# Kernel optimization log

Measured on AMD Instinct MI355X. Metric: run time of the kernel, lower is better.

The kernel has to match this reference:

```python
import jax, jax.numpy as jnp
from jax import lax
import numpy as np

WINDOW_SIZE = 11
SIGMA = 1.5
C1 = 0.01 ** 2
C2 = 0.03 ** 2


def _gauss_1d(n=WINDOW_SIZE, sigma=SIGMA):
    # replicates cv2.getGaussianKernel(n, sigma)
    x = np.arange(n, dtype=np.float64) - (n - 1) / 2.0
    g = np.exp(-(x ** 2) / (2.0 * sigma ** 2))
    return (g / g.sum()).astype(np.float32)


def _blur(x, g):
    """Separable 2D Gaussian blur of x [N,1,H,W]; math equals conv with g g^T."""
    p = g.shape[0] // 2
    kh = g.reshape(1, 1, -1, 1).astype(x.dtype)  # [O,I,KH,1]
    kw = g.reshape(1, 1, 1, -1).astype(x.dtype)  # [O,I,1,KW]
    dn = ('NCHW', 'OIHW', 'NCHW')
    x = lax.conv_general_dilated(x, kh, (1, 1), [(p, p), (0, 0)], dimension_numbers=dn)
    x = lax.conv_general_dilated(x, kw, (1, 1), [(0, 0), (p, p)], dimension_numbers=dn)
    return x


def _ssim_loss_2d(a, b):
    """a, b: [N,1,H,W]. Returns 1 - mean(SSIM map) with the module's exact formula."""
    g = jnp.asarray(_gauss_1d())
    mu1 = _blur(a, g)
    mu2 = _blur(b, g)
    mu1_sq = mu1 * mu1
    mu2_sq = mu2 * mu2
    mu1_mu2 = mu1 * mu2
    sigma1_sq = _blur(a * a, g) - mu1_sq
    sigma2_sq = _blur(b * b, g) - mu2_sq
    sigma12 = _blur(a * b, g) - mu1_mu2
    luminance = (2 * mu1_mu2 + C1) / (mu1_sq + mu2_sq + C1)
    contrast = (2 * sigma12 + C2) / (sigma1_sq + sigma2_sq + C2)
    structure = (sigma12 + C2) / (jnp.sqrt(sigma1_sq) * jnp.sqrt(sigma2_sq) + C2)
    ssim = luminance * contrast * structure
    return 1.0 - ssim.mean()


def setup_inputs() -> dict:
    key = jax.random.key(0)
    k1, k2, k3 = jax.random.split(key, 3)
    img1_3d = jax.random.uniform(k1, (4, 1, 16, 512, 512), dtype=jnp.float32)
    img1_2d = jax.random.uniform(k2, (4, 1, 512, 512), dtype=jnp.float32)
    img2 = jax.random.uniform(k3, (4, 1, 16, 512, 512), dtype=jnp.float32)
    return {"img1_3d": img1_3d, "img1_2d": img1_2d, "img2": img2}


def reference(img1_3d, img1_2d, img2):
    B, C, D, H, W = img1_3d.shape  # C == 1 (forced by groups=C with single-out-channel weight)
    # 3D SSIM: kernel depth 1, depth padding 0 -> per-slice 2D blur; fold D into batch.
    a3 = img1_3d.reshape(B * D, 1, H, W)
    b3 = img2.reshape(B * D, 1, H, W)
    loss3d = _ssim_loss_2d(a3, b3)
    # 2D SSIM against depth-averaged img2.
    b2 = jnp.mean(img2, axis=2)  # [B,1,H,W]
    loss2d = _ssim_loss_2d(img1_2d, b2)
    return loss3d + loss2d
```

## Files before the change

### kernel.cpp

```cpp
#include <hip/hip_runtime.h>
#include <cmath>


#define WSZ 11
#define IMG 512
#define SLICE (IMG * IMG)

typedef float f32x2 __attribute__((ext_vector_type(2)));
typedef float f32x4 __attribute__((ext_vector_type(4)));

struct G11 { float w[WSZ]; };

__global__ __launch_bounds__(256, 5)
void ssim_pk_kernel(const float* __restrict__ A3, const float* __restrict__ B3,
                    const float* __restrict__ A2, const float* __restrict__ B2,
                    double* __restrict__ acc, G11 gw)
{
    __shared__ f32x4 A4[2][262];
    __shared__ f32x4 B4[2][262];
    __shared__ f32x2 Z2[2][262];
    __shared__ float bsum[4];

    const int tx = threadIdx.x;
    const int x0 = tx * 2;

    const int unit = blockIdx.x;
    const float* Ap;
    const float* Bp;
    double* accp;
    int y0, TST;
    if (unit < 1536) {
        int slice = unit / 24;
        int band  = unit - slice * 24;
        Ap = A3 + (long)slice * SLICE;
        Bp = B3 + (long)slice * SLICE;
        accp = acc + 0;
        if (band < 16) { y0 = band * 22;              TST = 22 + 10; }
        else           { y0 = 352 + (band - 16) * 20; TST = 20 + 10; }
    } else {
        int uu = unit - 1536;
        int img  = uu >> 6;
        int band = uu & 63;
        Ap = A2 + (long)img * SLICE;
        Bp = B2 + (long)img * SLICE;
        accp = acc + 1;
        y0 = band * 8;
        TST = 8 + 10;
    }

    if (tx < 3) {
        f32x4 z4 = {0.f, 0.f, 0.f, 0.f};
        f32x2 z2 = {0.f, 0.f};
        A4[0][tx] = z4; A4[1][tx] = z4; A4[0][259 + tx] = z4; A4[1][259 + tx] = z4;
        B4[0][tx] = z4; B4[1][tx] = z4; B4[0][259 + tx] = z4; B4[1][259 + tx] = z4;
        Z2[0][tx] = z2; Z2[1][tx] = z2; Z2[0][259 + tx] = z2; Z2[1][259 + tx] = z2;
    }

    f32x2 ra[11], rb[11];
    #pragma unroll
    for (int i = 0; i < 11; i++) { ra[i] = (f32x2){0.f, 0.f}; rb[i] = (f32x2){0.f, 0.f}; }

    float sum = 0.f;

    f32x2 aN = {0.f, 0.f}, bN = {0.f, 0.f};
    {
        int r = y0 - 5;
        if (r >= 0 && r < IMG) {
            aN = *(const f32x2*)&Ap[(long)r * IMG + x0];
            bN = *(const f32x2*)&Bp[(long)r * IMG + x0];
        }
    }

    const f32x2 C1v = {1e-4f, 1e-4f};
    const f32x2 C2v = {9e-4f, 9e-4f};

    for (int t0 = 0; t0 < TST; t0 += 11) {
        #pragma unroll
        for (int u = 0; u < 11; u++) {
            const int t = t0 + u;
            if (t < TST) {
                ra[u] = aN;
                rb[u] = bN;

                {
                    int rn = y0 - 4 + t;
                    aN = (f32x2){0.f, 0.f}; bN = (f32x2){0.f, 0.f};
                    if ((t + 1 < TST) && rn >= 0 && rn < IMG) {
                        aN = *(const f32x2*)&Ap[(long)rn * IMG + x0];
                        bN = *(const f32x2*)&Bp[(long)rn * IMG + x0];
                    }
                }

                if (t >= 10) {
                    f32x2 m1 = {0.f, 0.f}, m2 = m1, xx = m1, yy = m1, zz = m1;
                    #pragma unroll
                    for (int j = 0; j < 11; j++) {
                        const int s = (u + 1 + j) % 11;
                        const f32x2 g2 = {gw.w[j], gw.w[j]};
                        f32x2 a = ra[s], b = rb[s];
                        f32x2 ga = g2 * a, gb = g2 * b;
                        m1 += ga; m2 += gb;
                        xx += ga * a; yy += gb * b; zz += ga * b;
                    }
                    const int buf = t & 1;
                    A4[buf][3 + tx] = __builtin_shufflevector(m1, m2, 0, 1, 2, 3);
                    B4[buf][3 + tx] = __builtin_shufflevector(xx, yy, 0, 1, 2, 3);
                    Z2[buf][3 + tx] = zz;
                    __syncthreads();

                    f32x2 OM1 = {0.f, 0.f}, OM2 = OM1, OXX = OM1, OYY = OM1, OZZ = OM1;
                    {
                        f32x4 pa = A4[buf][tx], pb = B4[buf][tx];
                        f32x2 pz = Z2[buf][tx];
                        const f32x2 c = {gw.w[0], 0.f};
                        OM1 += c * __builtin_shufflevector(pa, pa, 1, 1);
                        OM2 += c * __builtin_shufflevector(pa, pa, 3, 3);
                        OXX += c * __builtin_shufflevector(pb, pb, 1, 1);
                        OYY += c * __builtin_shufflevector(pb, pb, 3, 3);
                        OZZ += c * __builtin_shufflevector(pz, pz, 1, 1);
                    }
                    #pragma unroll
                    for (int jj = 1; jj <= 5; jj++) {
                        f32x4 pa = A4[buf][tx + jj], pb = B4[buf][tx + jj];
                        f32x2 pz = Z2[buf][tx + jj];
                        const f32x2 cA = {gw.w[2 * jj - 1], gw.w[2 * jj - 2]};
                        const f32x2 cB = {gw.w[2 * jj],     gw.w[2 * jj - 1]};
                        OM1 += cA * __builtin_shufflevector(pa, pa, 0, 0)
                             + cB * __builtin_shufflevector(pa, pa, 1, 1);
                        OM2 += cA * __builtin_shufflevector(pa, pa, 2, 2)
                             + cB * __builtin_shufflevector(pa, pa, 3, 3);
                        OXX += cA * __builtin_shufflevector(pb, pb, 0, 0)
                             + cB * __builtin_shufflevector(pb, pb, 1, 1);
                        OYY += cA * __builtin_shufflevector(pb, pb, 2, 2)
                             + cB * __builtin_shufflevector(pb, pb, 3, 3);
                        OZZ += cA * __builtin_shufflevector(pz, pz, 0, 0)
                             + cB * __builtin_shufflevector(pz, pz, 1, 1);
                    }
                    {
                        f32x4 pa = A4[buf][tx + 6], pb = B4[buf][tx + 6];
                        f32x2 pz = Z2[buf][tx + 6];
                        const f32x2 c = {0.f, gw.w[10]};
                        OM1 += c * __builtin_shufflevector(pa, pa, 0, 0);
                        OM2 += c * __builtin_shufflevector(pa, pa, 2, 2);
                        OXX += c * __builtin_shufflevector(pb, pb, 0, 0);
                        OYY += c * __builtin_shufflevector(pb, pb, 2, 2);
                        OZZ += c * __builtin_shufflevector(pz, pz, 0, 0);
                    }

                    f32x2 m1s = OM1 * OM1, m2s = OM2 * OM2, m12 = OM1 * OM2;
                    f32x2 s1 = OXX - m1s, s2 = OYY - m2s, s12 = OZZ - m12;
                    f32x2 d1 = m1s + m2s + C1v;
                    f32x2 d2 = s1 + s2 + C2v;
                    f32x2 num = (2.f * m12 + C1v) * (2.f * s12 + C2v) * (s12 + C2v);
                    float d3x = __builtin_amdgcn_sqrtf(s1.x) * __builtin_amdgcn_sqrtf(s2.x) + 9e-4f;
                    float d3y = __builtin_amdgcn_sqrtf(s1.y) * __builtin_amdgcn_sqrtf(s2.y) + 9e-4f;
                    sum += num.x * __builtin_amdgcn_rcpf(d1.x * d2.x * d3x);
                    sum += num.y * __builtin_amdgcn_rcpf(d1.y * d2.y * d3y);
                }
            }
        }
    }

    for (int off = 32; off > 0; off >>= 1)
        sum += __shfl_down(sum, off, 64);
    if ((tx & 63) == 0) bsum[tx >> 6] = sum;
    __syncthreads();
    if (tx == 0) {
        float tot = bsum[0] + bsum[1] + bsum[2] + bsum[3];
        atomicAdd(accp, (double)tot);
    }
}

__global__ __launch_bounds__(256) void depth_mean4_kernel(
    const float4* __restrict__ img2, float4* __restrict__ b2)
{
    const int per = SLICE / 4;
    int idx = blockIdx.x * 256 + threadIdx.x;
    int b = idx >> 16;
    int p = idx & (per - 1);
    const float4* src = img2 + (long)b * 16 * per + p;
    float sx = 0.f, sy = 0.f, sz = 0.f, sw = 0.f;
    #pragma unroll
    for (int d = 0; d < 16; d++) {
        float4 v = src[(long)d * per];
        sx += v.x; sy += v.y; sz += v.z; sw += v.w;
    }
    float4 o; o.x = sx * 0.0625f; o.y = sy * 0.0625f; o.z = sz * 0.0625f; o.w = sw * 0.0625f;
    b2[idx] = o;
}

__global__ void finalize_kernel(const double* __restrict__ acc, float* __restrict__ out)
{
    double loss3 = 1.0 - acc[0] / (64.0 * (double)SLICE);
    double loss2 = 1.0 - acc[1] / (4.0 * (double)SLICE);
    out[0] = (float)(loss3 + loss2);
}

extern "C" void kernel_launch(void* const* d_in, const int* in_sizes, int n_in,
                              void* d_out, int out_size, void* d_ws, size_t ws_size,
                              hipStream_t stream)
{
    const float* img1_3d = (const float*)d_in[0];
    const float* img1_2d = (const float*)d_in[1];
    const float* img2    = (const float*)d_in[2];
    float* out = (float*)d_out;

    double* acc = (double*)d_ws;
    float*  b2  = (float*)((char*)d_ws + 256);

    G11 gw;
    {
        double g[WSZ], s = 0.0;
        for (int i = 0; i < WSZ; i++) {
            double xx = (double)i - (WSZ - 1) / 2.0;
            g[i] = std::exp(-(xx * xx) / (2.0 * 1.5 * 1.5));
            s += g[i];
        }
        for (int i = 0; i < WSZ; i++) gw.w[i] = (float)(g[i] / s);
    }

    hipMemsetAsync(acc, 0, 2 * sizeof(double), stream);

    depth_mean4_kernel<<<(4 * SLICE / 4) / 256, 256, 0, stream>>>(
        (const float4*)img2, (float4*)b2);

    ssim_pk_kernel<<<1792, 256, 0, stream>>>(img1_3d, img2, img1_2d, b2, acc, gw);

    finalize_kernel<<<1, 1, 0, stream>>>(acc, out);
}
```

Measured before the change: 106.0 us.

## Make each wavefront own an independent column strip to drop block barriers

Restructures the SSIM kernel so each 64-lane wavefront processes its own 58-column output strip with 3-column halos, using per-wave shared buffers instead of a block-wide row. This removes the per-row __syncthreads and the double-buffered LDS, relying on intra-wavefront ordering of LDS accesses. The cost is redundant halo loads and compute (6 of 64 lanes produce no output) and more atomics, one per wave. Band partitioning for the 3D and 2D parts is also rebalanced.

```diff
diff --git a/kernel.cpp b/kernel.cpp
--- a/kernel.cpp
+++ b/kernel.cpp
@@ -12,48 +12,55 @@
 struct G11 { float w[WSZ]; };
 
 __global__ __launch_bounds__(256, 5)
-void ssim_pk_kernel(const float* __restrict__ A3, const float* __restrict__ B3,
+void ssim_ws_kernel(const float* __restrict__ A3, const float* __restrict__ B3,
                     const float* __restrict__ A2, const float* __restrict__ B2,
                     double* __restrict__ acc, G11 gw)
 {
-    __shared__ f32x4 A4[2][262];
-    __shared__ f32x4 B4[2][262];
-    __shared__ f32x2 Z2[2][262];
-    __shared__ float bsum[4];
-
-    const int tx = threadIdx.x;
-    const int x0 = tx * 2;
-
-    const int unit = blockIdx.x;
-    const float* Ap;
-    const float* Bp;
-    double* accp;
-    int y0, TST;
-    if (unit < 1536) {
-        int slice = unit / 24;
-        int band  = unit - slice * 24;
+    __shared__ f32x4 A4[4][70];
+    __shared__ f32x4 B4[4][70];
+    __shared__ f32x2 Z2[4][70];
+
+    const int tx   = threadIdx.x;
+    const int wid  = tx >> 6;
+    const int lane = tx & 63;
+
+    const int u = blockIdx.x * 4 + wid;
+    const float* Ap; const float* Bp; double* accp;
+    int y0, BND, strip;
+    if (u < 7680) {
+        int slice = u / 120;
+        int r = u - slice * 120;
+        int band = r / 5; strip = r - band * 5;
         Ap = A3 + (long)slice * SLICE;
         Bp = B3 + (long)slice * SLICE;
         accp = acc + 0;
-        if (band < 16) { y0 = band * 22;              TST = 22 + 10; }
-        else           { y0 = 352 + (band - 16) * 20; TST = 20 + 10; }
+        if (band < 8) { y0 = band * 22;              BND = 22; }
+        else          { y0 = 176 + (band - 8) * 21;  BND = 21; }
     } else {
-        int uu = unit - 1536;
-        int img  = uu >> 6;
-        int band = uu & 63;
+        int u2 = u - 7680;
+        int img = u2 / 130;
+        int r2 = u2 - img * 130;
+        int band = r2 / 5; strip = r2 - band * 5;
         Ap = A2 + (long)img * SLICE;
         Bp = B2 + (long)img * SLICE;
         accp = acc + 1;
-        y0 = band * 8;
-        TST = 8 + 10;
-    }
-
-    if (tx < 3) {
-        f32x4 z4 = {0.f, 0.f, 0.f, 0.f};
-        f32x2 z2 = {0.f, 0.f};
-        A4[0][tx] = z4; A4[1][tx] = z4; A4[0][259 + tx] = z4; A4[1][259 + tx] = z4;
-        B4[0][tx] = z4; B4[1][tx] = z4; B4[0][259 + tx] = z4; B4[1][259 + tx] = z4;
-        Z2[0][tx] = z2; Z2[1][tx] = z2; Z2[0][259 + tx] = z2; Z2[1][259 + tx] = z2;
+        if (band < 18) { y0 = band * 20;              BND = 20; }
+        else           { y0 = 360 + (band - 18) * 19; BND = 19; }
+    }
+    const int TST = BND + 10;
+    const int ip  = strip * 58 - 3 + lane;
+    const bool vin  = (ip >= 0) && (ip < 256);
+    const bool vout = (lane >= 3) && (lane <= 60) && (ip < 256);
+    const int x0 = 2 * ip;
+
+    if (lane < 3) {
+        A4[wid][lane] = (f32x4){0.f, 0.f, 0.f, 0.f};
+        B4[wid][lane] = (f32x4){0.f, 0.f, 0.f, 0.f};
+        Z2[wid][lane] = (f32x2){0.f, 0.f};
+    } else if (lane >= 61) {
+        A4[wid][lane + 6] = (f32x4){0.f, 0.f, 0.f, 0.f};
+        B4[wid][lane + 6] = (f32x4){0.f, 0.f, 0.f, 0.f};
+        Z2[wid][lane + 6] = (f32x2){0.f, 0.f};
     }
 
     f32x2 ra[11], rb[11];
@@ -65,7 +72,7 @@
     f32x2 aN = {0.f, 0.f}, bN = {0.f, 0.f};
     {
         int r = y0 - 5;
-        if (r >= 0 && r < IMG) {
+        if (r >= 0 && r < IMG && vin) {
             aN = *(const f32x2*)&Ap[(long)r * IMG + x0];
             bN = *(const f32x2*)&Bp[(long)r * IMG + x0];
         }
@@ -76,16 +83,16 @@
 
     for (int t0 = 0; t0 < TST; t0 += 11) {
         #pragma unroll
-        for (int u = 0; u < 11; u++) {
-            const int t = t0 + u;
+        for (int uu = 0; uu < 11; uu++) {
+            const int t = t0 + uu;
             if (t < TST) {
-                ra[u] = aN;
-                rb[u] = bN;
+                ra[uu] = aN;
+                rb[uu] = bN;
 
                 {
                     int rn = y0 - 4 + t;
                     aN = (f32x2){0.f, 0.f}; bN = (f32x2){0.f, 0.f};
-                    if ((t + 1 < TST) && rn >= 0 && rn < IMG) {
+                    if ((t + 1 < TST) && rn >= 0 && rn < IMG && vin) {
                         aN = *(const f32x2*)&Ap[(long)rn * IMG + x0];
                         bN = *(const f32x2*)&Bp[(long)rn * IMG + x0];
                     }
@@ -95,23 +102,21 @@
                     f32x2 m1 = {0.f, 0.f}, m2 = m1, xx = m1, yy = m1, zz = m1;
                     #pragma unroll
                     for (int j = 0; j < 11; j++) {
-                        const int s = (u + 1 + j) % 11;
+                        const int s = (uu + 1 + j) % 11;
                         const f32x2 g2 = {gw.w[j], gw.w[j]};
                         f32x2 a = ra[s], b = rb[s];
                         f32x2 ga = g2 * a, gb = g2 * b;
                         m1 += ga; m2 += gb;
                         xx += ga * a; yy += gb * b; zz += ga * b;
                     }
-                    const int buf = t & 1;
-                    A4[buf][3 + tx] = __builtin_shufflevector(m1, m2, 0, 1, 2, 3);
-                    B4[buf][3 + tx] = __builtin_shufflevector(xx, yy, 0, 1, 2, 3);
-                    Z2[buf][3 + tx] = zz;
-                    __syncthreads();
+                    A4[wid][lane + 3] = __builtin_shufflevector(m1, m2, 0, 1, 2, 3);
+                    B4[wid][lane + 3] = __builtin_shufflevector(xx, yy, 0, 1, 2, 3);
+                    Z2[wid][lane + 3] = zz;
 
                     f32x2 OM1 = {0.f, 0.f}, OM2 = OM1, OXX = OM1, OYY = OM1, OZZ = OM1;
                     {
-                        f32x4 pa = A4[buf][tx], pb = B4[buf][tx];
-                        f32x2 pz = Z2[buf][tx];
+                        f32x4 pa = A4[wid][lane], pb = B4[wid][lane];
+                        f32x2 pz = Z2[wid][lane];
                         const f32x2 c = {gw.w[0], 0.f};
                         OM1 += c * __builtin_shufflevector(pa, pa, 1, 1);
                         OM2 += c * __builtin_shufflevector(pa, pa, 3, 3);
@@ -121,8 +126,8 @@
                     }
                     #pragma unroll
                     for (int jj = 1; jj <= 5; jj++) {
-                        f32x4 pa = A4[buf][tx + jj], pb = B4[buf][tx + jj];
-                        f32x2 pz = Z2[buf][tx + jj];
+                        f32x4 pa = A4[wid][lane + jj], pb = B4[wid][lane + jj];
+                        f32x2 pz = Z2[wid][lane + jj];
                         const f32x2 cA = {gw.w[2 * jj - 1], gw.w[2 * jj - 2]};
                         const f32x2 cB = {gw.w[2 * jj],     gw.w[2 * jj - 1]};
                         OM1 += cA * __builtin_shufflevector(pa, pa, 0, 0)
@@ -137,8 +142,8 @@
                              + cB * __builtin_shufflevector(pz, pz, 1, 1);
                     }
                     {
-                        f32x4 pa = A4[buf][tx + 6], pb = B4[buf][tx + 6];
-                        f32x2 pz = Z2[buf][tx + 6];
+                        f32x4 pa = A4[wid][lane + 6], pb = B4[wid][lane + 6];
+                        f32x2 pz = Z2[wid][lane + 6];
                         const f32x2 c = {0.f, gw.w[10]};
                         OM1 += c * __builtin_shufflevector(pa, pa, 0, 0);
                         OM2 += c * __builtin_shufflevector(pa, pa, 2, 2);
@@ -154,8 +159,9 @@
                     f32x2 num = (2.f * m12 + C1v) * (2.f * s12 + C2v) * (s12 + C2v);
                     float d3x = __builtin_amdgcn_sqrtf(s1.x) * __builtin_amdgcn_sqrtf(s2.x) + 9e-4f;
                     float d3y = __builtin_amdgcn_sqrtf(s1.y) * __builtin_amdgcn_sqrtf(s2.y) + 9e-4f;
-                    sum += num.x * __builtin_amdgcn_rcpf(d1.x * d2.x * d3x);
-                    sum += num.y * __builtin_amdgcn_rcpf(d1.y * d2.y * d3y);
+                    float contrib = num.x * __builtin_amdgcn_rcpf(d1.x * d2.x * d3x)
+                                  + num.y * __builtin_amdgcn_rcpf(d1.y * d2.y * d3y);
+                    sum += vout ? contrib : 0.f;
                 }
             }
         }
@@ -163,12 +169,8 @@
 
     for (int off = 32; off > 0; off >>= 1)
         sum += __shfl_down(sum, off, 64);
-    if ((tx & 63) == 0) bsum[tx >> 6] = sum;
-    __syncthreads();
-    if (tx == 0) {
-        float tot = bsum[0] + bsum[1] + bsum[2] + bsum[3];
-        atomicAdd(accp, (double)tot);
-    }
+    if (lane == 0)
+        atomicAdd(accp, (double)sum);
 }
 
 __global__ __launch_bounds__(256) void depth_mean4_kernel(
@@ -224,7 +226,7 @@
     depth_mean4_kernel<<<(4 * SLICE / 4) / 256, 256, 0, stream>>>(
         (const float4*)img2, (float4*)b2);
 
-    ssim_pk_kernel<<<1792, 256, 0, stream>>>(img1_3d, img2, img1_2d, b2, acc, gw);
+    ssim_ws_kernel<<<2050, 256, 0, stream>>>(img1_3d, img2, img1_2d, b2, acc, gw);
 
     finalize_kernel<<<1, 1, 0, stream>>>(acc, out);
 }
```

Result: slower. 166.7 us (+57.3%).

## Fuse depth-mean into SSIM kernel and schedule 2D blocks first

Applied to the files above, without the earlier changes.

Removes the separate depth_mean kernel and its intermediate buffer. The 2D SSIM blocks now average the 16 depth slices of img2 on the fly for each row they load. Those blocks are moved to the front of the grid so their heavier loads start early and overlap with the 3D blocks. This saves a kernel launch and a write-then-read of the averaged image. In exchange, each 2D block issues 16x the B loads, and halo rows are re-averaged across overlapping bands.

```diff
diff --git a/kernel.cpp b/kernel.cpp
--- a/kernel.cpp
+++ b/kernel.cpp
@@ -13,7 +13,7 @@
 
 __global__ __launch_bounds__(256, 5)
 void ssim_pk_kernel(const float* __restrict__ A3, const float* __restrict__ B3,
-                    const float* __restrict__ A2, const float* __restrict__ B2,
+                    const float* __restrict__ A2,
                     double* __restrict__ acc, G11 gw)
 {
     __shared__ f32x4 A4[2][262];
@@ -25,28 +25,38 @@
     const int x0 = tx * 2;
 
     const int unit = blockIdx.x;
+    const bool m16 = (unit < 256);
     const float* Ap;
     const float* Bp;
     double* accp;
     int y0, TST;
-    if (unit < 1536) {
-        int slice = unit / 24;
-        int band  = unit - slice * 24;
+    if (m16) {
+        int img  = unit >> 6;
+        int band = unit & 63;
+        Ap = A2 + (long)img * SLICE;
+        Bp = B3 + (long)img * 16 * SLICE;
+        accp = acc + 1;
+        y0 = band * 8;
+        TST = 8 + 10;
+    } else {
+        int uu = unit - 256;
+        int slice = uu / 24;
+        int band  = uu - slice * 24;
         Ap = A3 + (long)slice * SLICE;
         Bp = B3 + (long)slice * SLICE;
         accp = acc + 0;
         if (band < 16) { y0 = band * 22;              TST = 22 + 10; }
         else           { y0 = 352 + (band - 16) * 20; TST = 20 + 10; }
-    } else {
-        int uu = unit - 1536;
-        int img  = uu >> 6;
-        int band = uu & 63;
-        Ap = A2 + (long)img * SLICE;
-        Bp = B2 + (long)img * SLICE;
-        accp = acc + 1;
-        y0 = band * 8;
-        TST = 8 + 10;
-    }
+    }
+
+    auto loadB = [&](int r) -> f32x2 {
+        if (!m16) return *(const f32x2*)&Bp[(long)r * IMG + x0];
+        f32x2 s = {0.f, 0.f};
+        #pragma unroll
+        for (int d = 0; d < 16; d++)
+            s += *(const f32x2*)&Bp[(long)d * SLICE + (long)r * IMG + x0];
+        return s * 0.0625f;
+    };
 
     if (tx < 3) {
         f32x4 z4 = {0.f, 0.f, 0.f, 0.f};
@@ -67,7 +77,7 @@
         int r = y0 - 5;
         if (r >= 0 && r < IMG) {
             aN = *(const f32x2*)&Ap[(long)r * IMG + x0];
-            bN = *(const f32x2*)&Bp[(long)r * IMG + x0];
+            bN = loadB(r);
         }
     }
 
@@ -87,7 +97,7 @@
                     aN = (f32x2){0.f, 0.f}; bN = (f32x2){0.f, 0.f};
                     if ((t + 1 < TST) && rn >= 0 && rn < IMG) {
                         aN = *(const f32x2*)&Ap[(long)rn * IMG + x0];
-                        bN = *(const f32x2*)&Bp[(long)rn * IMG + x0];
+                        bN = loadB(rn);
                     }
                 }
 
@@ -171,24 +181,6 @@
     }
 }
 
-__global__ __launch_bounds__(256) void depth_mean4_kernel(
-    const float4* __restrict__ img2, float4* __restrict__ b2)
-{
-    const int per = SLICE / 4;
-    int idx = blockIdx.x * 256 + threadIdx.x;
-    int b = idx >> 16;
-    int p = idx & (per - 1);
-    const float4* src = img2 + (long)b * 16 * per + p;
-    float sx = 0.f, sy = 0.f, sz = 0.f, sw = 0.f;
-    #pragma unroll
-    for (int d = 0; d < 16; d++) {
-        float4 v = src[(long)d * per];
-        sx += v.x; sy += v.y; sz += v.z; sw += v.w;
-    }
-    float4 o; o.x = sx * 0.0625f; o.y = sy * 0.0625f; o.z = sz * 0.0625f; o.w = sw * 0.0625f;
-    b2[idx] = o;
-}
-
 __global__ void finalize_kernel(const double* __restrict__ acc, float* __restrict__ out)
 {
     double loss3 = 1.0 - acc[0] / (64.0 * (double)SLICE);
@@ -206,7 +198,6 @@
     float* out = (float*)d_out;
 
     double* acc = (double*)d_ws;
-    float*  b2  = (float*)((char*)d_ws + 256);
 
     G11 gw;
     {
@@ -221,10 +212,7 @@
 
     hipMemsetAsync(acc, 0, 2 * sizeof(double), stream);
 
-    depth_mean4_kernel<<<(4 * SLICE / 4) / 256, 256, 0, stream>>>(
-        (const float4*)img2, (float4*)b2);
-
-    ssim_pk_kernel<<<1792, 256, 0, stream>>>(img1_3d, img2, img1_2d, b2, acc, gw);
+    ssim_pk_kernel<<<1792, 256, 0, stream>>>(img1_3d, img2, img1_2d, acc, gw);
 
     finalize_kernel<<<1, 1, 0, stream>>>(acc, out);
 }
```

Measured after the change: 122.9 us. +15.9%, slower.
